# Performance work log

Measured on AMD Instinct MI355X. Metric: run time of the kernel, lower is better.

## Reference

```python
import jax, jax.numpy as jnp
import numpy as np

M, K, N = 4096, 4096, 11008  # tokens, in_features, out_features
PACK = 8  # int4 nibbles per int32


def setup_inputs() -> dict:
    key = jax.random.key(0)
    k1, k2, k3, k4, k5 = jax.random.split(key, 5)
    x = jax.random.normal(k1, (M, K), dtype=jnp.float32)
    weights = jax.random.randint(k2, (N, K // PACK), 0, 2147483647, dtype=jnp.int32)
    # positive per-channel scales, small float zero offsets (GPTQ-style affine)
    scales = jax.random.uniform(k3, (N,), dtype=jnp.float32, minval=0.005, maxval=0.02)
    zeros = jax.random.normal(k4, (N,), dtype=jnp.float32) * 0.05
    bias = jax.random.normal(k5, (N,), dtype=jnp.float32) * 0.02
    return {"x": x, "weights": weights, "scales": scales, "zeros": zeros, "bias": bias}


def _unpack_int4(weights):
    # weights: [N, K//8] int32 -> nibbles [N, K] in [0, 15]
    shifts = jnp.arange(PACK, dtype=jnp.int32) * 4  # [8]
    nib = (weights[:, :, None] >> shifts[None, None, :]) & 0xF  # [N, K//8, 8]
    return nib.reshape(weights.shape[0], -1)  # [N, K]


def reference(x, weights, scales, zeros, bias):
    x_dtype = x.dtype
    xb = x.astype(jnp.bfloat16)
    q = _unpack_int4(weights).astype(jnp.bfloat16)  # [N, K]
    # dequant: w = q * scale + zero  (per output channel)
    w = q * scales.astype(jnp.bfloat16)[:, None] + zeros.astype(jnp.bfloat16)[:, None]
    out = jnp.einsum('mk,nk->mn', xb, w, preferred_element_type=jnp.float32)
    out = out + bias[None, :]
    return out.astype(x_dtype)
```

## Files before the change

kernel.cpp:

```cpp
#include <hip/hip_runtime.h>
#include <stdint.h>

#define MDIM 4096
#define KDIM 4096
#define NDIM 11008
#define KP   (KDIM/8)

typedef float  f32x4   __attribute__((ext_vector_type(4)));
typedef __bf16 bf16x8  __attribute__((ext_vector_type(8)));
typedef unsigned short u16x8 __attribute__((ext_vector_type(8)));
typedef int    i32x4   __attribute__((ext_vector_type(4)));
typedef int    i32x16  __attribute__((ext_vector_type(16)));
typedef char   c8x8    __attribute__((ext_vector_type(8)));
typedef char   c8x16   __attribute__((ext_vector_type(16)));

__device__ __forceinline__ unsigned short f2bf(float f) {
  uint32_t u = __builtin_bit_cast(uint32_t, f);
  u += 0x7FFFu + ((u >> 16) & 1u);
  return (unsigned short)(u >> 16);
}
__device__ __forceinline__ float bf2f(unsigned short h) {
  return __builtin_bit_cast(float, (uint32_t)h << 16);
}
__device__ __forceinline__ float bf16r(float f) { return bf2f(f2bf(f)); }

__device__ __forceinline__ void lds16(const void* g, void* l) {
  __builtin_amdgcn_global_load_lds(
      (const __attribute__((address_space(1))) unsigned int*)g,
      (__attribute__((address_space(3))) unsigned int*)l, 16, 0, 0);
}

__global__ __launch_bounds__(256) void repack_q_kernel(
    const uint32_t* __restrict__ wq, c8x8* __restrict__ Q8) {
  int idx = blockIdx.x * 256 + threadIdx.x;
  uint32_t w = wq[idx];
  c8x8 v;
#pragma unroll
  for (int j = 0; j < 8; ++j) v[j] = (char)((w >> (4 * j)) & 0xF);
  Q8[idx] = v;
}

__global__ __launch_bounds__(256) void quant_x_kernel(
    const float* __restrict__ x, c8x16* __restrict__ X8,
    float* __restrict__ delta, float* __restrict__ xsum) {
  __shared__ float red[256];
  const int row = blockIdx.x, t = threadIdx.x;
  const float4* xr = (const float4*)(x + (size_t)row * KDIM);
  float xb[16];
#pragma unroll
  for (int i = 0; i < 4; ++i) {
    float4 f = xr[t * 4 + i];
    xb[i * 4 + 0] = bf16r(f.x); xb[i * 4 + 1] = bf16r(f.y);
    xb[i * 4 + 2] = bf16r(f.z); xb[i * 4 + 3] = bf16r(f.w);
  }
  float mx = 0.f, sm = 0.f;
#pragma unroll
  for (int j = 0; j < 16; ++j) { mx = fmaxf(mx, fabsf(xb[j])); sm += xb[j]; }
  red[t] = mx; __syncthreads();
  for (int o = 128; o > 0; o >>= 1) {
    if (t < o) red[t] = fmaxf(red[t], red[t + o]);
    __syncthreads();
  }
  const float rmx = red[0];
  __syncthreads();
  red[t] = sm; __syncthreads();
  for (int o = 128; o > 0; o >>= 1) {
    if (t < o) red[t] += red[t + o];
    __syncthreads();
  }
  const float rsm = red[0];
  const float inv = (rmx > 0.f) ? 127.0f / rmx : 0.f;
  if (t == 0) {
    delta[row] = (rmx > 0.f) ? rmx / 127.0f : 0.f;
    xsum[row]  = rsm;
  }
  c8x16 q;
#pragma unroll
  for (int j = 0; j < 16; ++j) q[j] = (char)__float2int_rn(xb[j] * inv);
  X8[(size_t)row * 256 + t] = q;
}

__global__ __launch_bounds__(256, 1) void gemm_i8_kernel(
    const char* __restrict__ A8, const char* __restrict__ Q8,
    const float* __restrict__ delta, const float* __restrict__ xsum,
    const float* __restrict__ scales, const float* __restrict__ zeros,
    const float* __restrict__ bias, float* __restrict__ out) {
  __shared__ __align__(16) char smem[131072];

  const int tid  = threadIdx.x;
  const int lane = tid & 63;
  const int wave = tid >> 6;
  const int wm   = wave >> 1;
  const int wn   = wave & 1;

  const int b   = blockIdx.x;
  const int swz = (b & 7) * 86 + (b >> 3);
  const int mt  = swz / 43;
  const int nt  = swz - mt * 43;
  const int bm0 = mt * 256, bn0 = nt * 256;

  const int srow   = lane >> 2;
  const int schunk = lane & 3;
  const int p0c    = schunk ^ (((srow >> 3) & 1) << 1);
  const char* aRe = A8 + (size_t)(bm0 + wave * 64 + srow) * KDIM + (size_t)(p0c * 16);
  const char* aRo = A8 + (size_t)(bm0 + wave * 64 + srow) * KDIM + (size_t)((p0c ^ 1) * 16);
  const char* bRe = Q8 + (size_t)(bn0 + wave * 64 + srow) * KDIM + (size_t)(p0c * 16);
  const char* bRo = Q8 + (size_t)(bn0 + wave * 64 + srow) * KDIM + (size_t)((p0c ^ 1) * 16);

  const int r31 = lane & 31;
  const int sub = r31 >> 4;
  const int r15 = r31 & 15;
  const int hk  = lane >> 5;
  const int rd0 = sub * 1024 + r15 * 64 + ((hk ^ sub) << 4) + ((r15 & 8) << 2);
  const int rd1 = rd0 ^ 32;

  const int aoffc = wm * 8192;
  const int boffc = 65536 + wn * 8192;

  i32x16 acc[4][4];
#pragma unroll
  for (int i = 0; i < 4; ++i)
#pragma unroll
    for (int j = 0; j < 4; ++j)
#pragma unroll
      for (int r = 0; r < 16; ++r) acc[i][j][r] = 0;

  i32x4 Af[4], Bf[4];

#define ABASE(S) ((S) << 14)
#define BBASE(S) (65536 + ((S) << 14))

#define STAGE_A(tile, h, slot)                                              \
  do {                                                                      \
    const size_t ko_ = (size_t)((tile) * 128 + (h) * 64);                   \
    char* d_ = smem + ABASE(slot) + wave * 4096;                            \
    lds16(aRe + ko_,                        d_);                            \
    lds16(aRo + (size_t)16 * KDIM + ko_,    d_ + 1024);                     \
    lds16(aRe + (size_t)32 * KDIM + ko_,    d_ + 2048);                     \
    lds16(aRo + (size_t)48 * KDIM + ko_,    d_ + 3072);                     \
  } while (0)

#define STAGE_B(tile, h, slot)                                              \
  do {                                                                      \
    const size_t ko_ = (size_t)((tile) * 128 + (h) * 64);                   \
    char* d_ = smem + BBASE(slot) + wave * 4096;                            \
    lds16(bRe + ko_,                        d_);                            \
    lds16(bRo + (size_t)16 * KDIM + ko_,    d_ + 1024);                     \
    lds16(bRe + (size_t)32 * KDIM + ko_,    d_ + 2048);                     \
    lds16(bRo + (size_t)48 * KDIM + ko_,    d_ + 3072);                     \
  } while (0)

#define READ8(S, KS)                                                        \
  do {                                                                      \
    const int ro_ = (KS) ? rd1 : rd0;                                       \
    _Pragma("unroll") for (int mf = 0; mf < 4; ++mf)                        \
        Af[mf] = *(const i32x4*)(smem + aoffc + ABASE(S) +                  \
                                 mf * 2048 + ro_);                          \
    _Pragma("unroll") for (int nf = 0; nf < 4; ++nf)                        \
        Bf[nf] = *(const i32x4*)(smem + boffc + ((S) << 14) +               \
                                 nf * 2048 + ro_);                          \
  } while (0)

#define MFMA16()                                                            \
  __builtin_amdgcn_s_setprio(1);                                            \
  _Pragma("unroll") for (int mf = 0; mf < 4; ++mf)                          \
      _Pragma("unroll") for (int nf = 0; nf < 4; ++nf)                      \
          acc[mf][nf] = __builtin_amdgcn_mfma_i32_32x32x32_i8(              \
              Af[mf], Bf[nf], acc[mf][nf], 0, 0, 0);                        \
  __builtin_amdgcn_s_setprio(0);

#define BAR                                                                 \
  __builtin_amdgcn_s_barrier();                                             \
  __builtin_amdgcn_sched_barrier(0);

#define VMWAIT(N) asm volatile("s_waitcnt vmcnt(" #N ")" ::: "memory")

#define TILE(T, S0s, S1s, SN1s, NSTG, VM1STMT, VM3STMT)                     \
  do {                                                                      \
    READ8(S0s, 0);                                                          \
    if ((NSTG) >= 1) STAGE_A((T) + 1, 1, SN1s);                             \
    BAR; MFMA16(); BAR;                                                     \
    READ8(S0s, 1);                                                          \
    if ((NSTG) >= 2) STAGE_B((T) + 1, 1, SN1s);                             \
    VM1STMT;                                                                \
    BAR; MFMA16(); BAR;                                                     \
    READ8(S1s, 0);                                                          \
    if ((NSTG) >= 3) STAGE_A((T) + 2, 0, S0s);                              \
    BAR; MFMA16(); BAR;                                                     \
    READ8(S1s, 1);                                                          \
    if ((NSTG) >= 4) STAGE_B((T) + 2, 0, S0s);                              \
    VM3STMT;                                                                \
    BAR; MFMA16(); BAR;                                                     \
  } while (0)

  STAGE_A(0, 0, 0); STAGE_B(0, 0, 0);
  STAGE_A(0, 1, 1); STAGE_B(0, 1, 1);
  STAGE_A(1, 0, 2); STAGE_B(1, 0, 2);
  VMWAIT(16);
  BAR;

  for (int tt = 0; tt < 30; tt += 2) {
    TILE(tt,     0, 1, 3, 4, VMWAIT(16), VMWAIT(16));
    TILE(tt + 1, 2, 3, 1, 4, VMWAIT(16), VMWAIT(16));
  }
  TILE(30, 0, 1, 3, 2, VMWAIT(16), VMWAIT(8));
  TILE(31, 2, 3, 1, 0, VMWAIT(0), (void)0);

#undef TILE
#undef VMWAIT
#undef BAR
#undef MFMA16
#undef READ8
#undef STAGE_B
#undef STAGE_A
#undef BBASE
#undef ABASE

  const int colv = bn0 + wn * 128 + (lane & 31);
  const int rowb = bm0 + wm * 128 + ((lane >> 5) << 2);
  float sb[4], zb[4], bv[4];
#pragma unroll
  for (int nf = 0; nf < 4; ++nf) {
    sb[nf] = bf16r(scales[colv + nf * 32]);
    zb[nf] = bf16r(zeros[colv + nf * 32]);
    bv[nf] = bias[colv + nf * 32];
  }
#pragma unroll
  for (int mf = 0; mf < 4; ++mf)
#pragma unroll
    for (int reg = 0; reg < 16; ++reg) {
      const int row = rowb + mf * 32 + (reg & 3) + ((reg >> 2) << 3);
      const float dm = delta[row];
      const float xm = xsum[row];
#pragma unroll
      for (int nf = 0; nf < 4; ++nf)
        out[(size_t)row * NDIM + colv + nf * 32] =
            (float)acc[mf][nf][reg] * (dm * sb[nf]) + (zb[nf] * xm + bv[nf]);
    }
}

__global__ __launch_bounds__(256, 3) void gemm_fused_kernel(
    const float* __restrict__ x, const uint32_t* __restrict__ wq,
    const float* __restrict__ scales, const float* __restrict__ zeros,
    const float* __restrict__ bias, float* __restrict__ out) {
  __shared__ __align__(16) char smem[2 * 128 * 64 * 2];
  char* As = smem;
  char* Bs = smem + 16384;

  const int tid  = threadIdx.x;
  const int lane = tid & 63;
  const int wave = tid >> 6;
  const int wm = wave >> 1, wn = wave & 1;

  const int b   = blockIdx.x;
  const int swz = (b & 7) * 344 + (b >> 3);
  const int mt  = swz / 86;
  const int nt  = swz - mt * 86;
  const int bm0 = mt * 128, bn0 = nt * 128;

  f32x4 acc[4][4];
#pragma unroll
  for (int i = 0; i < 4; ++i)
#pragma unroll
    for (int j = 0; j < 4; ++j) acc[i][j] = (f32x4){0.f, 0.f, 0.f, 0.f};

  const int base_a = ((wm * 64 + (lane & 15)) << 7) + ((lane >> 4) << 4);
  const int base_b = ((wn * 64 + (lane & 15)) << 7) + ((lane >> 4) << 4);

  float sv[4], zv[4];
#pragma unroll
  for (int it = 0; it < 4; ++it) {
    int r = bn0 + it * 32 + (tid >> 3);
    sv[it] = bf16r(scales[r]);
    zv[it] = bf16r(zeros[r]);
  }

  for (int kt = 0; kt < KDIM / 64; ++kt) {
    const int k0 = kt * 64;
    __syncthreads();
#pragma unroll
    for (int it = 0; it < 4; ++it) {
      int ch = it * 256 + tid;
      int row = ch >> 3, c8 = ch & 7;
      const float* src = x + (size_t)(bm0 + row) * KDIM + k0 + c8 * 8;
      float4 f0 = *(const float4*)src;
      float4 f1 = *(const float4*)(src + 4);
      u16x8 v;
      v[0] = f2bf(f0.x); v[1] = f2bf(f0.y); v[2] = f2bf(f0.z); v[3] = f2bf(f0.w);
      v[4] = f2bf(f1.x); v[5] = f2bf(f1.y); v[6] = f2bf(f1.z); v[7] = f2bf(f1.w);
      *(u16x8*)(As + row * 128 + c8 * 16) = v;
    }
#pragma unroll
    for (int it = 0; it < 4; ++it) {
      int ch = it * 256 + tid;
      int row = ch >> 3, kp = ch & 7;
      uint32_t w = wq[(size_t)(bn0 + row) * KP + kt * 8 + kp];
      float s = sv[it], z = zv[it];
      u16x8 v;
#pragma unroll
      for (int j = 0; j < 8; ++j) {
        float qf = (float)((w >> (4 * j)) & 0xF);
        float t  = bf16r(qf * s);
        v[j] = f2bf(t + z);
      }
      *(u16x8*)(Bs + row * 128 + kp * 16) = v;
    }
    __syncthreads();
#pragma unroll
    for (int ks = 0; ks < 2; ++ks) {
      bf16x8 af[4], bf[4];
#pragma unroll
      for (int i = 0; i < 4; ++i)
        af[i] = *(const bf16x8*)(As + base_a + i * 2048 + ks * 64);
#pragma unroll
      for (int j = 0; j < 4; ++j)
        bf[j] = *(const bf16x8*)(Bs + base_b + j * 2048 + ks * 64);
#pragma unroll
      for (int i = 0; i < 4; ++i)
#pragma unroll
        for (int j = 0; j < 4; ++j)
          acc[i][j] = __builtin_amdgcn_mfma_f32_16x16x32_bf16(af[i], bf[j],
                                                              acc[i][j], 0, 0, 0);
    }
  }

  const int colbase = bn0 + wn * 64 + (lane & 15);
  const int rowbase = bm0 + wm * 64 + ((lane >> 4) << 2);
  float bv[4];
#pragma unroll
  for (int j = 0; j < 4; ++j) bv[j] = bias[colbase + j * 16];
#pragma unroll
  for (int i = 0; i < 4; ++i) {
#pragma unroll
    for (int j = 0; j < 4; ++j) {
      size_t base = (size_t)(rowbase + i * 16) * NDIM + colbase + j * 16;
#pragma unroll
      for (int r = 0; r < 4; ++r)
        out[base + (size_t)r * NDIM] = acc[i][j][r] + bv[j];
    }
  }
}

extern "C" void kernel_launch(void* const* d_in, const int* in_sizes, int n_in,
                              void* d_out, int out_size, void* d_ws, size_t ws_size,
                              hipStream_t stream) {
  const float*    x      = (const float*)d_in[0];
  const uint32_t* wq     = (const uint32_t*)d_in[1];
  const float*    scales = (const float*)d_in[2];
  const float*    zeros  = (const float*)d_in[3];
  const float*    bias   = (const float*)d_in[4];
  float*          out    = (float*)d_out;

  const size_t offQ = 0;
  const size_t szQ  = (size_t)NDIM * KDIM;
  const size_t offX = szQ;
  const size_t szX  = (size_t)MDIM * KDIM;
  const size_t offD = offX + szX;
  const size_t offS = offD + MDIM * sizeof(float);
  const size_t need = offS + MDIM * sizeof(float);

  if (ws_size >= need) {
    char*  Q8    = (char*)d_ws + offQ;
    char*  X8    = (char*)d_ws + offX;
    float* dlt   = (float*)((char*)d_ws + offD);
    float* xsm   = (float*)((char*)d_ws + offS);
    repack_q_kernel<<<(NDIM * KP) / 256, 256, 0, stream>>>(wq, (c8x8*)Q8);
    quant_x_kernel<<<MDIM, 256, 0, stream>>>(x, (c8x16*)X8, dlt, xsm);
    gemm_i8_kernel<<<688, 256, 0, stream>>>(X8, Q8, dlt, xsm, scales, zeros,
                                            bias, out);
  } else {
    gemm_fused_kernel<<<2752, 256, 0, stream>>>(x, wq, scales, zeros, bias, out);
  }
}
```

Before: 234.2 us.

## Give each wave private LDS staging to drop workgroup barriers

Each wave now loads its own 128-row A and B slices into a private 32KB LDS region with double buffering, so the k-loop needs no workgroup barriers, only per-wave vmcnt waits. This removes the barrier stalls between MFMA phases that came from cooperative staging. In exchange, A and B rows are loaded redundantly by waves that share them (two waves per slice), which doubles global/L2 traffic per block, and the prefetch depth drops to one tile.

Result: slower. 262.7 us (+12.2%).

```diff
diff --git a/kernel.cpp b/kernel.cpp
--- a/kernel.cpp
+++ b/kernel.cpp
@@ -102,10 +102,10 @@
   const int srow   = lane >> 2;
   const int schunk = lane & 3;
   const int p0c    = schunk ^ (((srow >> 3) & 1) << 1);
-  const char* aRe = A8 + (size_t)(bm0 + wave * 64 + srow) * KDIM + (size_t)(p0c * 16);
-  const char* aRo = A8 + (size_t)(bm0 + wave * 64 + srow) * KDIM + (size_t)((p0c ^ 1) * 16);
-  const char* bRe = Q8 + (size_t)(bn0 + wave * 64 + srow) * KDIM + (size_t)(p0c * 16);
-  const char* bRo = Q8 + (size_t)(bn0 + wave * 64 + srow) * KDIM + (size_t)((p0c ^ 1) * 16);
+  const char* aE = A8 + (size_t)(bm0 + wm * 128 + srow) * KDIM + (size_t)(p0c * 16);
+  const char* aO = A8 + (size_t)(bm0 + wm * 128 + srow) * KDIM + (size_t)((p0c ^ 1) * 16);
+  const char* bE = Q8 + (size_t)(bn0 + wn * 128 + srow) * KDIM + (size_t)(p0c * 16);
+  const char* bO = Q8 + (size_t)(bn0 + wn * 128 + srow) * KDIM + (size_t)((p0c ^ 1) * 16);
 
   const int r31 = lane & 31;
   const int sub = r31 >> 4;
@@ -114,8 +114,7 @@
   const int rd0 = sub * 1024 + r15 * 64 + ((hk ^ sub) << 4) + ((r15 & 8) << 2);
   const int rd1 = rd0 ^ 32;
 
-  const int aoffc = wm * 8192;
-  const int boffc = 65536 + wn * 8192;
+  const int wbase = wave << 15;
 
   i32x16 acc[4][4];
 #pragma unroll
@@ -127,38 +126,27 @@
 
   i32x4 Af[4], Bf[4];
 
-#define ABASE(S) ((S) << 14)
-#define BBASE(S) (65536 + ((S) << 14))
-
-#define STAGE_A(tile, h, slot)                                              \
+#define STAGE_AB(t, slot)                                                   \
   do {                                                                      \
-    const size_t ko_ = (size_t)((tile) * 128 + (h) * 64);                   \
-    char* d_ = smem + ABASE(slot) + wave * 4096;                            \
-    lds16(aRe + ko_,                        d_);                            \
-    lds16(aRo + (size_t)16 * KDIM + ko_,    d_ + 1024);                     \
-    lds16(aRe + (size_t)32 * KDIM + ko_,    d_ + 2048);                     \
-    lds16(aRo + (size_t)48 * KDIM + ko_,    d_ + 3072);                     \
+    const size_t ko_ = (size_t)(t) * 64;                                    \
+    char* da_ = smem + wbase + (slot) * 16384;                              \
+    char* db_ = da_ + 8192;                                                 \
+    _Pragma("unroll") for (int j = 0; j < 8; ++j) {                         \
+      lds16(((j & 1) ? aO : aE) + (size_t)j * 16 * KDIM + ko_,              \
+            da_ + j * 1024);                                                \
+      lds16(((j & 1) ? bO : bE) + (size_t)j * 16 * KDIM + ko_,              \
+            db_ + j * 1024);                                                \
+    }                                                                       \
   } while (0)
 
-#define STAGE_B(tile, h, slot)                                              \
-  do {                                                                      \
-    const size_t ko_ = (size_t)((tile) * 128 + (h) * 64);                   \
-    char* d_ = smem + BBASE(slot) + wave * 4096;                            \
-    lds16(bRe + ko_,                        d_);                            \
-    lds16(bRo + (size_t)16 * KDIM + ko_,    d_ + 1024);                     \
-    lds16(bRe + (size_t)32 * KDIM + ko_,    d_ + 2048);                     \
-    lds16(bRo + (size_t)48 * KDIM + ko_,    d_ + 3072);                     \
-  } while (0)
-
-#define READ8(S, KS)                                                        \
+#define READ8(slot, KS)                                                     \
   do {                                                                      \
     const int ro_ = (KS) ? rd1 : rd0;                                       \
+    const int sb_ = wbase + (slot) * 16384;                                 \
     _Pragma("unroll") for (int mf = 0; mf < 4; ++mf)                        \
-        Af[mf] = *(const i32x4*)(smem + aoffc + ABASE(S) +                  \
-                                 mf * 2048 + ro_);                          \
+        Af[mf] = *(const i32x4*)(smem + sb_ + mf * 2048 + ro_);             \
     _Pragma("unroll") for (int nf = 0; nf < 4; ++nf)                        \
-        Bf[nf] = *(const i32x4*)(smem + boffc + ((S) << 14) +               \
-                                 nf * 2048 + ro_);                          \
+        Bf[nf] = *(const i32x4*)(smem + sb_ + 8192 + nf * 2048 + ro_);      \
   } while (0)
 
 #define MFMA16()                                                            \
@@ -169,52 +157,36 @@
               Af[mf], Bf[nf], acc[mf][nf], 0, 0, 0);                        \
   __builtin_amdgcn_s_setprio(0);
 
-#define BAR                                                                 \
-  __builtin_amdgcn_s_barrier();                                             \
-  __builtin_amdgcn_sched_barrier(0);
+#define BODY(slot)                                                          \
+  do {                                                                      \
+    READ8(slot, 0);                                                         \
+    MFMA16();                                                               \
+    READ8(slot, 1);                                                         \
+    MFMA16();                                                               \
+  } while (0)
 
 #define VMWAIT(N) asm volatile("s_waitcnt vmcnt(" #N ")" ::: "memory")
 
-#define TILE(T, S0s, S1s, SN1s, NSTG, VM1STMT, VM3STMT)                     \
-  do {                                                                      \
-    READ8(S0s, 0);                                                          \
-    if ((NSTG) >= 1) STAGE_A((T) + 1, 1, SN1s);                             \
-    BAR; MFMA16(); BAR;                                                     \
-    READ8(S0s, 1);                                                          \
-    if ((NSTG) >= 2) STAGE_B((T) + 1, 1, SN1s);                             \
-    VM1STMT;                                                                \
-    BAR; MFMA16(); BAR;                                                     \
-    READ8(S1s, 0);                                                          \
-    if ((NSTG) >= 3) STAGE_A((T) + 2, 0, S0s);                              \
-    BAR; MFMA16(); BAR;                                                     \
-    READ8(S1s, 1);                                                          \
-    if ((NSTG) >= 4) STAGE_B((T) + 2, 0, S0s);                              \
-    VM3STMT;                                                                \
-    BAR; MFMA16(); BAR;                                                     \
-  } while (0)
-
-  STAGE_A(0, 0, 0); STAGE_B(0, 0, 0);
-  STAGE_A(0, 1, 1); STAGE_B(0, 1, 1);
-  STAGE_A(1, 0, 2); STAGE_B(1, 0, 2);
+  STAGE_AB(0, 0);
+  for (int tt = 0; tt < 62; tt += 2) {
+    STAGE_AB(tt + 1, 1);
+    VMWAIT(16);
+    BODY(0);
+    STAGE_AB(tt + 2, 0);
+    VMWAIT(16);
+    BODY(1);
+  }
+  STAGE_AB(63, 1);
   VMWAIT(16);
-  BAR;
-
-  for (int tt = 0; tt < 30; tt += 2) {
-    TILE(tt,     0, 1, 3, 4, VMWAIT(16), VMWAIT(16));
-    TILE(tt + 1, 2, 3, 1, 4, VMWAIT(16), VMWAIT(16));
-  }
-  TILE(30, 0, 1, 3, 2, VMWAIT(16), VMWAIT(8));
-  TILE(31, 2, 3, 1, 0, VMWAIT(0), (void)0);
-
-#undef TILE
+  BODY(0);
+  VMWAIT(0);
+  BODY(1);
+
 #undef VMWAIT
-#undef BAR
+#undef BODY
 #undef MFMA16
 #undef READ8
-#undef STAGE_B
-#undef STAGE_A
-#undef BBASE
-#undef ABASE
+#undef STAGE_AB
 
   const int colv = bn0 + wn * 128 + (lane & 31);
   const int rowb = bm0 + wm * 128 + ((lane >> 5) << 2);
```
